# Performance work log

Hardware: AMD Instinct MI355X
Metric: run time of the kernel (lower is better)

The kernel has to match this reference:

```python
import jax, jax.numpy as jnp
import numpy as np

B, L, D_MODEL, H, H_DIM = 2, 4096, 768, 1, 128
D_K = H * H_DIM
F_LEN = L // 2 + 1
TEMP = 1.0
EPS = 1e-9
INV_SQRT_DK = float(1.0 / np.sqrt(H_DIM))


def _selector(xc, W1, b1, W2, b2, noise, temp):
    # xc: [B, h, d, F] complex. torch view_as_real(x.transpose(-1,-2))[..., 0] == real part.
    xr = jnp.real(jnp.swapaxes(xc, -1, -2))          # [B, h, F, d]
    h1 = jax.nn.relu(xr @ W1.T + b1)                 # [B, h, F, d//2]
    logit = h1 @ W2.T + b2                           # [B, h, F, 2]
    g = -jnp.log(-jnp.log(noise + EPS) + EPS)        # gumbel noise from uniform input
    z = jax.nn.softmax((logit + g) / temp, axis=-1)[..., 1]  # training mode: soft mask
    return z[..., None, :]                           # [B, h, 1, F]


def _forward(query, key, mask, Wq, bq, Wk, bk, qW1, qb1, qW2, qb2, kW1, kb1, kW2, kb2, q_noise, k_noise):
    nb, Lq = query.shape[0], query.shape[1]
    q = (query @ Wq.T + bq).reshape(nb, Lq, H, H_DIM).transpose(0, 2, 3, 1)  # [B, h, d, L]
    k = (key @ Wk.T + bk).reshape(nb, Lq, H, H_DIM).transpose(0, 2, 3, 1)
    q_tff = jnp.fft.rfft(q, axis=-1)                 # [B, h, d, F] complex
    k_tff = jnp.fft.rfft(k, axis=-1)
    q_m = _selector(q_tff, qW1, qb1, qW2, qb2, q_noise, TEMP)
    k_m = _selector(k_tff, kW1, kb1, kW2, kb2, k_noise, TEMP)
    qf = jnp.fft.irfft(q_tff * q_m, n=Lq, axis=-1)   # [B, h, d, L]
    kf = jnp.fft.irfft(k_tff * k_m, n=Lq, axis=-1)
    scores = jnp.einsum('bhdl,bhdm->bhlm', qf, kf) * INV_SQRT_DK  # [B, h, L, L]
    m = mask[:, None, :, :Lq]                        # [B, 1, 1, L]
    scores = jnp.where(m == 0, -1e9, scores)
    return jax.nn.softmax(scores, axis=-1)           # dropout omitted (eval/identity)


def setup_inputs() -> dict:
    key = jax.random.key(0)
    ks = jax.random.split(key, 12)
    s = 0.02
    return {
        'query': jax.random.normal(ks[0], (B, L, D_MODEL), jnp.float32),
        'key': jax.random.normal(ks[1], (B, L, D_MODEL), jnp.float32),
        'mask': jax.random.randint(ks[2], (B, 1, L), 0, 2, jnp.int32),
        'Wq': s * jax.random.normal(ks[3], (D_K, D_MODEL), jnp.float32),
        'bq': jnp.zeros((D_K,), jnp.float32),
        'Wk': s * jax.random.normal(ks[4], (D_K, D_MODEL), jnp.float32),
        'bk': jnp.zeros((D_K,), jnp.float32),
        'qW1': s * jax.random.normal(ks[5], (D_K // 2, D_K), jnp.float32),
        'qb1': jnp.zeros((D_K // 2,), jnp.float32),
        'qW2': s * jax.random.normal(ks[6], (2, D_K // 2), jnp.float32),
        'qb2': jnp.zeros((2,), jnp.float32),
        'kW1': s * jax.random.normal(ks[7], (D_K // 2, D_K), jnp.float32),
        'kb1': jnp.zeros((D_K // 2,), jnp.float32),
        'kW2': s * jax.random.normal(ks[8], (2, D_K // 2), jnp.float32),
        'kb2': jnp.zeros((2,), jnp.float32),
        'q_noise': jax.random.uniform(ks[9], (B, H, F_LEN, 2), jnp.float32),
        'k_noise': jax.random.uniform(ks[10], (B, H, F_LEN, 2), jnp.float32),
    }


def reference(query, key, mask, Wq, bq, Wk, bk, qW1, qb1, qW2, qb2, kW1, kb1, kW2, kb2, q_noise, k_noise):
    return _forward(query, key, mask, Wq, bq, Wk, bk, qW1, qb1, qW2, qb2, kW1, kb1, kW2, kb2, q_noise, k_noise)
```

## Files before the change

### kernel.cpp

```cpp
#include <hip/hip_runtime.h>
#include <hip/hip_bf16.h>

#define LL 4096
#define FL 2049
#define DKN 128
#define DMOD 768

#define TW_OFF   0
#define XT_OFF   4096
#define SPEC_OFF (4096 + 2097152)
#define Z_OFF    (SPEC_OFF + 2098176)

using bf16x8 = __attribute__((ext_vector_type(8))) short;
using f32x4  = __attribute__((ext_vector_type(4))) float;

__device__ __forceinline__ float2 cmul(float2 a, float2 b) {
    return make_float2(a.x * b.x - a.y * b.y, a.x * b.y + a.y * b.x);
}
__device__ __forceinline__ int SWZ(int a) { return a ^ ((a >> 4) & 15); }
__device__ __forceinline__ ushort f2bf(float f) {
    __hip_bfloat16 h = __float2bfloat16(f);
    return *(ushort*)&h;
}

__global__ void k_twiddle(float2* __restrict__ tw) {
    int j = blockIdx.x * 256 + threadIdx.x;
    if (j < 2048) {
        double a = -2.0 * 3.14159265358979323846 * (double)j / 4096.0;
        tw[j] = make_float2((float)cos(a), (float)sin(a));
    }
}

__global__ __launch_bounds__(256) void k_gemm1(const float* __restrict__ X,
                                               const float* __restrict__ W,
                                               const float* __restrict__ bias,
                                               float* __restrict__ out) {
    __shared__ float sX[16][64];
    __shared__ float sW[16][64];
    int b  = blockIdx.z;
    int l0 = blockIdx.x * 64;
    int d0 = blockIdx.y * 64;
    int t  = threadIdx.x;
    int lid = t >> 2, kq = (t & 3) * 4;
    int tx = t & 15, ty = t >> 4;
    const float* Xb = X + (size_t)b * LL * DMOD;
    float acc[4][4] = {};
    for (int k0 = 0; k0 < DMOD; k0 += 16) {
        float4 xv = *(const float4*)&Xb[(size_t)(l0 + lid) * DMOD + k0 + kq];
        float4 wv = *(const float4*)&W[(size_t)(d0 + lid) * DMOD + k0 + kq];
        sX[kq + 0][lid] = xv.x; sX[kq + 1][lid] = xv.y; sX[kq + 2][lid] = xv.z; sX[kq + 3][lid] = xv.w;
        sW[kq + 0][lid] = wv.x; sW[kq + 1][lid] = wv.y; sW[kq + 2][lid] = wv.z; sW[kq + 3][lid] = wv.w;
        __syncthreads();
#pragma unroll
        for (int k = 0; k < 16; k++) {
            float4 a = *(const float4*)&sX[k][tx * 4];
            float4 w = *(const float4*)&sW[k][ty * 4];
            acc[0][0] = fmaf(a.x, w.x, acc[0][0]); acc[0][1] = fmaf(a.x, w.y, acc[0][1]);
            acc[0][2] = fmaf(a.x, w.z, acc[0][2]); acc[0][3] = fmaf(a.x, w.w, acc[0][3]);
            acc[1][0] = fmaf(a.y, w.x, acc[1][0]); acc[1][1] = fmaf(a.y, w.y, acc[1][1]);
            acc[1][2] = fmaf(a.y, w.z, acc[1][2]); acc[1][3] = fmaf(a.y, w.w, acc[1][3]);
            acc[2][0] = fmaf(a.z, w.x, acc[2][0]); acc[2][1] = fmaf(a.z, w.y, acc[2][1]);
            acc[2][2] = fmaf(a.z, w.z, acc[2][2]); acc[2][3] = fmaf(a.z, w.w, acc[2][3]);
            acc[3][0] = fmaf(a.w, w.x, acc[3][0]); acc[3][1] = fmaf(a.w, w.y, acc[3][1]);
            acc[3][2] = fmaf(a.w, w.z, acc[3][2]); acc[3][3] = fmaf(a.w, w.w, acc[3][3]);
        }
        __syncthreads();
    }
#pragma unroll
    for (int j = 0; j < 4; j++) {
        int d = d0 + ty * 4 + j;
        float bb = bias[d];
        float4 r = make_float4(acc[0][j] + bb, acc[1][j] + bb, acc[2][j] + bb, acc[3][j] + bb);
        *(float4*)&out[((size_t)(b * DKN + d)) * LL + l0 + tx * 4] = r;
    }
}

template <int INV>
__global__ __launch_bounds__(512) void k_fft4(const float* __restrict__ xin,
                                              float2* __restrict__ spec,
                                              const float* __restrict__ zsel,
                                              float* __restrict__ xout,
                                              const float2* __restrict__ tw) {
    __shared__ float2 buf[4096];
    int ser = blockIdx.x;
    int t   = threadIdx.x;
    if (!INV) {
        const float* x = xin + (size_t)ser * LL;
        for (int i = t; i < 4096; i += 512) buf[SWZ(i)] = make_float2(x[i], 0.f);
    } else {
        const float2* sp = spec + (size_t)ser * FL;
        const float*  zz = zsel + (size_t)(ser >> 7) * FL;
        for (int f = t; f < FL; f += 512) {
            float2 v = sp[f];
            float  m = zz[f];
            float2 vm = make_float2(v.x * m, v.y * m);
            buf[SWZ(f)] = vm;
            if (f > 0 && f < 2048) buf[SWZ(4096 - f)] = make_float2(vm.x, -vm.y);
        }
    }
    __syncthreads();
#pragma unroll
    for (int st = 0; st < 6; st++) {
        int Lm1 = (1 << (2 * st)) - 1;
        float2 x0[2], x1[2], x2[2], x3[2];
#pragma unroll
        for (int ii = 0; ii < 2; ii++) {
            int idx = t + 512 * ii;
            x0[ii] = buf[SWZ(idx)];
            x1[ii] = buf[SWZ(idx + 1024)];
            x2[ii] = buf[SWZ(idx + 2048)];
            x3[ii] = buf[SWZ(idx + 3072)];
        }
        __syncthreads();
#pragma unroll
        for (int ii = 0; ii < 2; ii++) {
            int idx = t + 512 * ii;
            int q = idx & Lm1;
            int r = idx - q;
            int wbase = q + (r << 2);
            int L = Lm1 + 1;
            float2 a0 = x0[ii], a1 = x1[ii], a2 = x2[ii], a3 = x3[ii];
            float2 t0 = make_float2(a0.x + a2.x, a0.y + a2.y);
            float2 t1 = make_float2(a0.x - a2.x, a0.y - a2.y);
            float2 t2 = make_float2(a1.x + a3.x, a1.y + a3.y);
            float2 t3 = make_float2(a1.x - a3.x, a1.y - a3.y);
            float2 y0 = make_float2(t0.x + t2.x, t0.y + t2.y);
            float2 y2 = make_float2(t0.x - t2.x, t0.y - t2.y);
            float2 y1, y3;
            if (!INV) {
                y1 = make_float2(t1.x + t3.y, t1.y - t3.x);
                y3 = make_float2(t1.x - t3.y, t1.y + t3.x);
            } else {
                y1 = make_float2(t1.x - t3.y, t1.y + t3.x);
                y3 = make_float2(t1.x + t3.y, t1.y - t3.x);
            }
            float2 w1 = tw[r];
            float2 w2 = tw[2 * r];
            if (INV) { w1.y = -w1.y; w2.y = -w2.y; }
            float2 w3 = cmul(w1, w2);
            buf[SWZ(wbase)]         = y0;
            buf[SWZ(wbase + L)]     = cmul(y1, w1);
            buf[SWZ(wbase + 2 * L)] = cmul(y2, w2);
            buf[SWZ(wbase + 3 * L)] = cmul(y3, w3);
        }
        __syncthreads();
    }
    if (!INV) {
        float2* sp = spec + (size_t)ser * FL;
        for (int f = t; f < FL; f += 512) sp[f] = buf[SWZ(f)];
    } else {
        float* xo = xout + (size_t)ser * LL;
        const float sc = 1.0f / 4096.0f;
        for (int i = t; i < 4096; i += 512) xo[i] = buf[SWZ(i)].x * sc;
    }
}

__global__ __launch_bounds__(64) void k_selector(const float2* __restrict__ spec,
                                                 const float* __restrict__ W1,
                                                 const float* __restrict__ b1,
                                                 const float* __restrict__ W2,
                                                 const float* __restrict__ b2,
                                                 const float* __restrict__ noise,
                                                 float* __restrict__ z,
                                                 int tensor) {
    int f = blockIdx.x;
    int b = blockIdx.y;
    int j = threadIdx.x;
    __shared__ __align__(16) float xr[128];
    const float2* sp = spec + (size_t)(tensor * 2 + b) * DKN * FL;
    xr[j]      = sp[(size_t)j * FL + f].x;
    xr[j + 64] = sp[(size_t)(j + 64) * FL + f].x;
    __syncthreads();
    float acc = b1[j];
    const float4* w4 = (const float4*)&W1[(size_t)j * 128];
    const float4* x4 = (const float4*)xr;
#pragma unroll
    for (int d4 = 0; d4 < 32; d4++) {
        float4 w = w4[d4];
        float4 x = x4[d4];
        acc = fmaf(x.x, w.x, acc);
        acc = fmaf(x.y, w.y, acc);
        acc = fmaf(x.z, w.z, acc);
        acc = fmaf(x.w, w.w, acc);
    }
    float h = fmaxf(acc, 0.f);
    float l0 = h * W2[j];
    float l1 = h * W2[64 + j];
#pragma unroll
    for (int off = 32; off >= 1; off >>= 1) {
        l0 += __shfl_down(l0, off);
        l1 += __shfl_down(l1, off);
    }
    if (j == 0) {
        l0 += b2[0];
        l1 += b2[1];
        const float* nz = noise + ((size_t)b * FL + f) * 2;
        float g0 = -logf(-logf(nz[0] + 1e-9f) + 1e-9f);
        float g1 = -logf(-logf(nz[1] + 1e-9f) + 1e-9f);
        float a0 = l0 + g0, a1 = l1 + g1;
        z[(size_t)(tensor * 2 + b) * FL + f] = 1.f / (1.f + expf(a0 - a1));
    }
}

__global__ __launch_bounds__(256) void k_tr(const float* __restrict__ xt,
                                            ushort* __restrict__ xtb) {
    __shared__ float s[64][129];
    int tb = blockIdx.y;
    int l0 = blockIdx.x * 64;
    int t  = threadIdx.x;
    const float* g = xt + (size_t)tb * DKN * LL;
    int d = t >> 1, c0 = (t & 1) * 32;
#pragma unroll
    for (int j4 = 0; j4 < 8; j4++) {
        float4 v = *(const float4*)&g[(size_t)d * LL + l0 + c0 + j4 * 4];
        s[c0 + j4 * 4 + 0][d] = v.x;
        s[c0 + j4 * 4 + 1][d] = v.y;
        s[c0 + j4 * 4 + 2][d] = v.z;
        s[c0 + j4 * 4 + 3][d] = v.w;
    }
    __syncthreads();
    int l = t >> 2, dc0 = (t & 3) * 32;
    ushort* o = xtb + (size_t)tb * LL * DKN + (size_t)(l0 + l) * DKN + dc0;
#pragma unroll
    for (int c8 = 0; c8 < 4; c8++) {
        union { ushort us[8]; uint4 v; } pk;
#pragma unroll
        for (int u = 0; u < 8; u++) pk.us[u] = f2bf(s[l][dc0 + c8 * 8 + u]);
        *(uint4*)&o[c8 * 8] = pk.v;
    }
}

__global__ __launch_bounds__(256) void k_scores_mfma(const ushort* __restrict__ xtb,
                                                     float* __restrict__ out) {
    int b  = blockIdx.z;
    int m0 = blockIdx.x * 128;
    int l0 = blockIdx.y * 128;
    int wid  = threadIdx.x >> 6;
    int lane = threadIdx.x & 63;
    int wr = wid >> 1, wc = wid & 1;
    const ushort* A = xtb + (size_t)b * LL * DKN;
    const ushort* B = xtb + (size_t)(2 + b) * LL * DKN;
    int arow = l0 + wr * 64 + (lane & 15);
    int brow = m0 + wc * 64 + (lane & 15);
    int kcol = (lane >> 4) * 8;
    f32x4 acc[4][4] = {};
#pragma unroll
    for (int kk = 0; kk < 4; kk++) {
        bf16x8 af[4], bf[4];
#pragma unroll
        for (int mt = 0; mt < 4; mt++)
            af[mt] = *(const bf16x8*)&A[(size_t)(arow + mt * 16) * DKN + kk * 32 + kcol];
#pragma unroll
        for (int nt = 0; nt < 4; nt++)
            bf[nt] = *(const bf16x8*)&B[(size_t)(brow + nt * 16) * DKN + kk * 32 + kcol];
#pragma unroll
        for (int mt = 0; mt < 4; mt++)
#pragma unroll
            for (int nt = 0; nt < 4; nt++)
                acc[mt][nt] = __builtin_amdgcn_mfma_f32_16x16x32_bf16(af[mt], bf[nt], acc[mt][nt], 0, 0, 0);
    }
    const float sc = 0.08838834764831843f;
    int rg = lane >> 4, cl = lane & 15;
#pragma unroll
    for (int mt = 0; mt < 4; mt++) {
#pragma unroll
        for (int r = 0; r < 4; r++) {
            int l = l0 + wr * 64 + mt * 16 + rg * 4 + r;
            float* orow = out + ((size_t)(b * LL + l)) * LL + m0 + wc * 64 + cl;
#pragma unroll
            for (int nt = 0; nt < 4; nt++)
                orow[nt * 16] = acc[mt][nt][r] * sc;
        }
    }
}

__global__ __launch_bounds__(256) void k_softmax(float* __restrict__ out,
                                                 const int* __restrict__ mask) {
    int row = blockIdx.x;
    int b   = row >> 12;
    float* p = out + (size_t)row * LL;
    const int* mk = mask + (size_t)b * LL;
    int t = threadIdx.x;
    float4 v[4];
    int4   mv[4];
    float mx = -3.0e38f;
#pragma unroll
    for (int c = 0; c < 4; c++) {
        int base = c * 1024 + t * 4;
        v[c]  = *(const float4*)&p[base];
        mv[c] = *(const int4*)&mk[base];
        if (mv[c].x) mx = fmaxf(mx, v[c].x);
        if (mv[c].y) mx = fmaxf(mx, v[c].y);
        if (mv[c].z) mx = fmaxf(mx, v[c].z);
        if (mv[c].w) mx = fmaxf(mx, v[c].w);
    }
    __shared__ float redm[4], reds[4];
    int wid = t >> 6, lane = t & 63;
#pragma unroll
    for (int off = 32; off >= 1; off >>= 1) mx = fmaxf(mx, __shfl_xor(mx, off));
    if (lane == 0) redm[wid] = mx;
    __syncthreads();
    mx = fmaxf(fmaxf(redm[0], redm[1]), fmaxf(redm[2], redm[3]));
    float sum = 0.f;
#pragma unroll
    for (int c = 0; c < 4; c++) {
        v[c].x = mv[c].x ? expf(v[c].x - mx) : 0.f;
        v[c].y = mv[c].y ? expf(v[c].y - mx) : 0.f;
        v[c].z = mv[c].z ? expf(v[c].z - mx) : 0.f;
        v[c].w = mv[c].w ? expf(v[c].w - mx) : 0.f;
        sum += v[c].x + v[c].y + v[c].z + v[c].w;
    }
#pragma unroll
    for (int off = 32; off >= 1; off >>= 1) sum += __shfl_xor(sum, off);
    if (lane == 0) reds[wid] = sum;
    __syncthreads();
    sum = reds[0] + reds[1] + reds[2] + reds[3];
    float inv = 1.0f / sum;
#pragma unroll
    for (int c = 0; c < 4; c++) {
        int base = c * 1024 + t * 4;
        float4 r = make_float4(v[c].x * inv, v[c].y * inv, v[c].z * inv, v[c].w * inv);
        *(float4*)&p[base] = r;
    }
}

extern "C" void kernel_launch(void* const* d_in, const int* in_sizes, int n_in,
                              void* d_out, int out_size, void* d_ws, size_t ws_size,
                              hipStream_t stream) {
    (void)in_sizes; (void)n_in; (void)out_size; (void)ws_size;
    const float* query  = (const float*)d_in[0];
    const float* key    = (const float*)d_in[1];
    const int*   mask   = (const int*)d_in[2];
    const float* Wq     = (const float*)d_in[3];
    const float* bq     = (const float*)d_in[4];
    const float* Wk     = (const float*)d_in[5];
    const float* bk     = (const float*)d_in[6];
    const float* qW1    = (const float*)d_in[7];
    const float* qb1    = (const float*)d_in[8];
    const float* qW2    = (const float*)d_in[9];
    const float* qb2    = (const float*)d_in[10];
    const float* kW1    = (const float*)d_in[11];
    const float* kb1    = (const float*)d_in[12];
    const float* kW2    = (const float*)d_in[13];
    const float* kb2    = (const float*)d_in[14];
    const float* qnoise = (const float*)d_in[15];
    const float* knoise = (const float*)d_in[16];

    float*  ws   = (float*)d_ws;
    float2* tw   = (float2*)(ws + TW_OFF);
    float*  xt   = ws + XT_OFF;
    float2* spec = (float2*)(ws + SPEC_OFF);
    ushort* xtb  = (ushort*)(ws + SPEC_OFF);
    float*  zsel = ws + Z_OFF;
    float*  out  = (float*)d_out;

    k_twiddle<<<dim3(8), dim3(256), 0, stream>>>(tw);
    k_gemm1<<<dim3(64, 2, 2), dim3(256), 0, stream>>>(query, Wq, bq, xt);
    k_gemm1<<<dim3(64, 2, 2), dim3(256), 0, stream>>>(key, Wk, bk, xt + (size_t)2 * DKN * LL);
    k_fft4<0><<<dim3(512), dim3(512), 0, stream>>>(xt, spec, nullptr, nullptr, tw);
    k_selector<<<dim3(FL, 2), dim3(64), 0, stream>>>(spec, qW1, qb1, qW2, qb2, qnoise, zsel, 0);
    k_selector<<<dim3(FL, 2), dim3(64), 0, stream>>>(spec, kW1, kb1, kW2, kb2, knoise, zsel, 1);
    k_fft4<1><<<dim3(512), dim3(512), 0, stream>>>(nullptr, spec, zsel, xt, tw);
    k_tr<<<dim3(64, 4), dim3(256), 0, stream>>>(xt, xtb);
    k_scores_mfma<<<dim3(32, 32, 2), dim3(256), 0, stream>>>(xtb, out);
    k_softmax<<<dim3(8192), dim3(256), 0, stream>>>(out, mask);
}
```

Baseline: 404.4 us.

## Fuse scores with online softmax and use split-bf16 MFMA for projections

The QK^T score computation and the masked softmax become one kernel. It computes an online max/sum in a first pass, then recomputes the scores in a second pass and writes normalized probabilities directly. This removes the write-then-read of the full 2x4096x4096 fp32 score matrix, at the cost of doing the QK^T MFMA work twice. Separately, the fp32 input projections now run on bf16 MFMA using a hi/lo split (three products per tile), which adds conversion kernels and extra workspace traffic for the hi/lo copies.

```diff
diff --git a/kernel.cpp b/kernel.cpp
--- a/kernel.cpp
+++ b/kernel.cpp
@@ -10,6 +10,10 @@
 #define XT_OFF   4096
 #define SPEC_OFF (4096 + 2097152)
 #define Z_OFF    (SPEC_OFF + 2098176)
+#define QKH_OFF  4207624
+#define QKL_OFF  (QKH_OFF + 6291456)
+#define WH_OFF   (QKL_OFF + 6291456)
+#define WL_OFF   (WH_OFF + 98304)
 
 using bf16x8 = __attribute__((ext_vector_type(8))) short;
 using f32x4  = __attribute__((ext_vector_type(4))) float;
@@ -21,6 +25,10 @@
 __device__ __forceinline__ ushort f2bf(float f) {
     __hip_bfloat16 h = __float2bfloat16(f);
     return *(ushort*)&h;
+}
+__device__ __forceinline__ float bf2f(ushort u) {
+    __hip_bfloat16 h = *(__hip_bfloat16*)&u;
+    return __bfloat162float(h);
 }
 
 __global__ void k_twiddle(float2* __restrict__ tw) {
@@ -31,48 +39,76 @@
     }
 }
 
-__global__ __launch_bounds__(256) void k_gemm1(const float* __restrict__ X,
-                                               const float* __restrict__ W,
-                                               const float* __restrict__ bias,
-                                               float* __restrict__ out) {
-    __shared__ float sX[16][64];
-    __shared__ float sW[16][64];
-    int b  = blockIdx.z;
+__global__ __launch_bounds__(256) void k_cvt(const float* __restrict__ src,
+                                             ushort* __restrict__ hi,
+                                             ushort* __restrict__ lo, int n) {
+    int i8 = (blockIdx.x * 256 + threadIdx.x) * 8;
+    if (i8 >= n) return;
+    float4 a = *(const float4*)&src[i8];
+    float4 b = *(const float4*)&src[i8 + 4];
+    float v[8] = {a.x, a.y, a.z, a.w, b.x, b.y, b.z, b.w};
+    union { ushort us[8]; uint4 q; } ph, pl;
+#pragma unroll
+    for (int u = 0; u < 8; u++) {
+        ushort h = f2bf(v[u]);
+        ph.us[u] = h;
+        pl.us[u] = f2bf(v[u] - bf2f(h));
+    }
+    *(uint4*)&hi[i8] = ph.q;
+    *(uint4*)&lo[i8] = pl.q;
+}
+
+__global__ __launch_bounds__(256) void k_proj(const ushort* __restrict__ XH,
+                                              const ushort* __restrict__ XL,
+                                              const ushort* __restrict__ WH,
+                                              const ushort* __restrict__ WL,
+                                              const float* __restrict__ bq,
+                                              const float* __restrict__ bk,
+                                              float* __restrict__ xt) {
+    int tz = blockIdx.z, b = blockIdx.y;
     int l0 = blockIdx.x * 64;
-    int d0 = blockIdx.y * 64;
-    int t  = threadIdx.x;
-    int lid = t >> 2, kq = (t & 3) * 4;
-    int tx = t & 15, ty = t >> 4;
-    const float* Xb = X + (size_t)b * LL * DMOD;
-    float acc[4][4] = {};
-    for (int k0 = 0; k0 < DMOD; k0 += 16) {
-        float4 xv = *(const float4*)&Xb[(size_t)(l0 + lid) * DMOD + k0 + kq];
-        float4 wv = *(const float4*)&W[(size_t)(d0 + lid) * DMOD + k0 + kq];
-        sX[kq + 0][lid] = xv.x; sX[kq + 1][lid] = xv.y; sX[kq + 2][lid] = xv.z; sX[kq + 3][lid] = xv.w;
-        sW[kq + 0][lid] = wv.x; sW[kq + 1][lid] = wv.y; sW[kq + 2][lid] = wv.z; sW[kq + 3][lid] = wv.w;
-        __syncthreads();
-#pragma unroll
-        for (int k = 0; k < 16; k++) {
-            float4 a = *(const float4*)&sX[k][tx * 4];
-            float4 w = *(const float4*)&sW[k][ty * 4];
-            acc[0][0] = fmaf(a.x, w.x, acc[0][0]); acc[0][1] = fmaf(a.x, w.y, acc[0][1]);
-            acc[0][2] = fmaf(a.x, w.z, acc[0][2]); acc[0][3] = fmaf(a.x, w.w, acc[0][3]);
-            acc[1][0] = fmaf(a.y, w.x, acc[1][0]); acc[1][1] = fmaf(a.y, w.y, acc[1][1]);
-            acc[1][2] = fmaf(a.y, w.z, acc[1][2]); acc[1][3] = fmaf(a.y, w.w, acc[1][3]);
-            acc[2][0] = fmaf(a.z, w.x, acc[2][0]); acc[2][1] = fmaf(a.z, w.y, acc[2][1]);
-            acc[2][2] = fmaf(a.z, w.z, acc[2][2]); acc[2][3] = fmaf(a.z, w.w, acc[2][3]);
-            acc[3][0] = fmaf(a.w, w.x, acc[3][0]); acc[3][1] = fmaf(a.w, w.y, acc[3][1]);
-            acc[3][2] = fmaf(a.w, w.z, acc[3][2]); acc[3][3] = fmaf(a.w, w.w, acc[3][3]);
-        }
-        __syncthreads();
-    }
-#pragma unroll
-    for (int j = 0; j < 4; j++) {
-        int d = d0 + ty * 4 + j;
-        float bb = bias[d];
-        float4 r = make_float4(acc[0][j] + bb, acc[1][j] + bb, acc[2][j] + bb, acc[3][j] + bb);
-        *(float4*)&out[((size_t)(b * DKN + d)) * LL + l0 + tx * 4] = r;
-    }
+    int t = threadIdx.x, w = t >> 6, lane = t & 63;
+    int g = lane >> 4, c = lane & 15;
+    size_t xrow0 = ((size_t)(tz * 2 + b)) * LL + l0;
+    const ushort* WHt = WH + (size_t)tz * DKN * DMOD;
+    const ushort* WLt = WL + (size_t)tz * DKN * DMOD;
+    const float* bias = tz ? bk : bq;
+    float* outp = xt + (size_t)(tz * 2 + b) * DKN * LL;
+    f32x4 acc[2][4] = {};
+    for (int ks = 0; ks < 24; ks++) {
+        int kb = ks * 32 + g * 8;
+        bf16x8 ah[2], al[2], xh[4], xl[4];
+#pragma unroll
+        for (int dt = 0; dt < 2; dt++) {
+            size_t ro = (size_t)(w * 32 + dt * 16 + c) * DMOD + kb;
+            ah[dt] = *(const bf16x8*)&WHt[ro];
+            al[dt] = *(const bf16x8*)&WLt[ro];
+        }
+#pragma unroll
+        for (int nt = 0; nt < 4; nt++) {
+            size_t ro = (xrow0 + nt * 16 + c) * DMOD + kb;
+            xh[nt] = *(const bf16x8*)&XH[ro];
+            xl[nt] = *(const bf16x8*)&XL[ro];
+        }
+#pragma unroll
+        for (int dt = 0; dt < 2; dt++)
+#pragma unroll
+            for (int nt = 0; nt < 4; nt++) {
+                acc[dt][nt] = __builtin_amdgcn_mfma_f32_16x16x32_bf16(ah[dt], xh[nt], acc[dt][nt], 0, 0, 0);
+                acc[dt][nt] = __builtin_amdgcn_mfma_f32_16x16x32_bf16(ah[dt], xl[nt], acc[dt][nt], 0, 0, 0);
+                acc[dt][nt] = __builtin_amdgcn_mfma_f32_16x16x32_bf16(al[dt], xh[nt], acc[dt][nt], 0, 0, 0);
+            }
+    }
+#pragma unroll
+    for (int dt = 0; dt < 2; dt++)
+#pragma unroll
+        for (int r = 0; r < 4; r++) {
+            int d = w * 32 + dt * 16 + g * 4 + r;
+            float bd = bias[d];
+#pragma unroll
+            for (int nt = 0; nt < 4; nt++)
+                outp[(size_t)d * LL + l0 + nt * 16 + c] = acc[dt][nt][r] + bd;
+        }
 }
 
 template <int INV>
@@ -208,11 +244,11 @@
     int tb = blockIdx.y;
     int l0 = blockIdx.x * 64;
     int t  = threadIdx.x;
-    const float* g = xt + (size_t)tb * DKN * LL;
+    const float* gp = xt + (size_t)tb * DKN * LL;
     int d = t >> 1, c0 = (t & 1) * 32;
 #pragma unroll
     for (int j4 = 0; j4 < 8; j4++) {
-        float4 v = *(const float4*)&g[(size_t)d * LL + l0 + c0 + j4 * 4];
+        float4 v = *(const float4*)&gp[(size_t)d * LL + l0 + c0 + j4 * 4];
         s[c0 + j4 * 4 + 0][d] = v.x;
         s[c0 + j4 * 4 + 1][d] = v.y;
         s[c0 + j4 * 4 + 2][d] = v.z;
@@ -230,97 +266,140 @@
     }
 }
 
-__global__ __launch_bounds__(256) void k_scores_mfma(const ushort* __restrict__ xtb,
+__global__ __launch_bounds__(256) void k_scores_soft(const ushort* __restrict__ xtb,
+                                                     const int* __restrict__ mask,
                                                      float* __restrict__ out) {
-    int b  = blockIdx.z;
-    int m0 = blockIdx.x * 128;
-    int l0 = blockIdx.y * 128;
-    int wid  = threadIdx.x >> 6;
-    int lane = threadIdx.x & 63;
-    int wr = wid >> 1, wc = wid & 1;
+    int b  = blockIdx.y;
+    int l0 = blockIdx.x * 32;
+    int t = threadIdx.x, w = t >> 6, lane = t & 63;
+    int g = lane >> 4, c = lane & 15;
     const ushort* A = xtb + (size_t)b * LL * DKN;
     const ushort* B = xtb + (size_t)(2 + b) * LL * DKN;
-    int arow = l0 + wr * 64 + (lane & 15);
-    int brow = m0 + wc * 64 + (lane & 15);
-    int kcol = (lane >> 4) * 8;
-    f32x4 acc[4][4] = {};
-#pragma unroll
-    for (int kk = 0; kk < 4; kk++) {
-        bf16x8 af[4], bf[4];
-#pragma unroll
-        for (int mt = 0; mt < 4; mt++)
-            af[mt] = *(const bf16x8*)&A[(size_t)(arow + mt * 16) * DKN + kk * 32 + kcol];
-#pragma unroll
-        for (int nt = 0; nt < 4; nt++)
-            bf[nt] = *(const bf16x8*)&B[(size_t)(brow + nt * 16) * DKN + kk * 32 + kcol];
-#pragma unroll
-        for (int mt = 0; mt < 4; mt++)
+    const int* mk = mask + (size_t)b * LL;
+    const float sc = 0.08838834764831843f;
+    bf16x8 af[2][4];
+#pragma unroll
+    for (int lt = 0; lt < 2; lt++)
+#pragma unroll
+        for (int kk = 0; kk < 4; kk++)
+            af[lt][kk] = *(const bf16x8*)&A[(size_t)(l0 + lt * 16 + c) * DKN + kk * 32 + g * 8];
+    float rM[2][4], rS[2][4];
+#pragma unroll
+    for (int lt = 0; lt < 2; lt++)
+#pragma unroll
+        for (int r = 0; r < 4; r++) { rM[lt][r] = -3.0e38f; rS[lt][r] = 0.f; }
+    for (int mt = 0; mt < 16; mt++) {
+        int m0 = w * 1024 + mt * 64;
+        f32x4 acc[2][4] = {};
+#pragma unroll
+        for (int kk = 0; kk < 4; kk++) {
+            bf16x8 bfr[4];
 #pragma unroll
             for (int nt = 0; nt < 4; nt++)
-                acc[mt][nt] = __builtin_amdgcn_mfma_f32_16x16x32_bf16(af[mt], bf[nt], acc[mt][nt], 0, 0, 0);
-    }
-    const float sc = 0.08838834764831843f;
-    int rg = lane >> 4, cl = lane & 15;
-#pragma unroll
-    for (int mt = 0; mt < 4; mt++) {
+                bfr[nt] = *(const bf16x8*)&B[(size_t)(m0 + nt * 16 + c) * DKN + kk * 32 + g * 8];
+#pragma unroll
+            for (int lt = 0; lt < 2; lt++)
+#pragma unroll
+                for (int nt = 0; nt < 4; nt++)
+                    acc[lt][nt] = __builtin_amdgcn_mfma_f32_16x16x32_bf16(af[lt][kk], bfr[nt], acc[lt][nt], 0, 0, 0);
+        }
+        int mv[4];
+#pragma unroll
+        for (int nt = 0; nt < 4; nt++) mv[nt] = mk[m0 + nt * 16 + c];
+#pragma unroll
+        for (int lt = 0; lt < 2; lt++)
+#pragma unroll
+            for (int r = 0; r < 4; r++) {
+                float sv[4];
+                float vmax = -3.0e38f;
+#pragma unroll
+                for (int nt = 0; nt < 4; nt++) {
+                    float s = mv[nt] ? acc[lt][nt][r] * sc : -1.0e9f;
+                    sv[nt] = s;
+                    vmax = fmaxf(vmax, s);
+                }
+                float nm = fmaxf(rM[lt][r], vmax);
+                float ssum = 0.f;
+#pragma unroll
+                for (int nt = 0; nt < 4; nt++) ssum += __expf(sv[nt] - nm);
+                rS[lt][r] = rS[lt][r] * __expf(rM[lt][r] - nm) + ssum;
+                rM[lt][r] = nm;
+            }
+    }
+#pragma unroll
+    for (int lt = 0; lt < 2; lt++)
 #pragma unroll
         for (int r = 0; r < 4; r++) {
-            int l = l0 + wr * 64 + mt * 16 + rg * 4 + r;
-            float* orow = out + ((size_t)(b * LL + l)) * LL + m0 + wc * 64 + cl;
+            float M = rM[lt][r], S = rS[lt][r];
+#pragma unroll
+            for (int off = 1; off < 16; off <<= 1) {
+                float om = __shfl_xor(M, off);
+                float os = __shfl_xor(S, off);
+                float nm = fmaxf(M, om);
+                S = S * __expf(M - nm) + os * __expf(om - nm);
+                M = nm;
+            }
+            rM[lt][r] = M; rS[lt][r] = S;
+        }
+    __shared__ float smM[4][32], smS[4][32];
+    if (c == 0) {
+#pragma unroll
+        for (int lt = 0; lt < 2; lt++)
+#pragma unroll
+            for (int r = 0; r < 4; r++) {
+                smM[w][lt * 16 + g * 4 + r] = rM[lt][r];
+                smS[w][lt * 16 + g * 4 + r] = rS[lt][r];
+            }
+    }
+    __syncthreads();
+    float Mf[2][4], Iv[2][4];
+#pragma unroll
+    for (int lt = 0; lt < 2; lt++)
+#pragma unroll
+        for (int r = 0; r < 4; r++) {
+            int row = lt * 16 + g * 4 + r;
+            float M = -3.0e38f, S = 0.f;
+#pragma unroll
+            for (int ww = 0; ww < 4; ww++) {
+                float om = smM[ww][row];
+                float os = smS[ww][row];
+                float nm = fmaxf(M, om);
+                S = S * __expf(M - nm) + os * __expf(om - nm);
+                M = nm;
+            }
+            Mf[lt][r] = M;
+            Iv[lt][r] = 1.0f / S;
+        }
+    for (int mt = 0; mt < 16; mt++) {
+        int m0 = w * 1024 + mt * 64;
+        f32x4 acc[2][4] = {};
+#pragma unroll
+        for (int kk = 0; kk < 4; kk++) {
+            bf16x8 bfr[4];
 #pragma unroll
             for (int nt = 0; nt < 4; nt++)
-                orow[nt * 16] = acc[mt][nt][r] * sc;
-        }
-    }
-}
-
-__global__ __launch_bounds__(256) void k_softmax(float* __restrict__ out,
-                                                 const int* __restrict__ mask) {
-    int row = blockIdx.x;
-    int b   = row >> 12;
-    float* p = out + (size_t)row * LL;
-    const int* mk = mask + (size_t)b * LL;
-    int t = threadIdx.x;
-    float4 v[4];
-    int4   mv[4];
-    float mx = -3.0e38f;
-#pragma unroll
-    for (int c = 0; c < 4; c++) {
-        int base = c * 1024 + t * 4;
-        v[c]  = *(const float4*)&p[base];
-        mv[c] = *(const int4*)&mk[base];
-        if (mv[c].x) mx = fmaxf(mx, v[c].x);
-        if (mv[c].y) mx = fmaxf(mx, v[c].y);
-        if (mv[c].z) mx = fmaxf(mx, v[c].z);
-        if (mv[c].w) mx = fmaxf(mx, v[c].w);
-    }
-    __shared__ float redm[4], reds[4];
-    int wid = t >> 6, lane = t & 63;
-#pragma unroll
-    for (int off = 32; off >= 1; off >>= 1) mx = fmaxf(mx, __shfl_xor(mx, off));
-    if (lane == 0) redm[wid] = mx;
-    __syncthreads();
-    mx = fmaxf(fmaxf(redm[0], redm[1]), fmaxf(redm[2], redm[3]));
-    float sum = 0.f;
-#pragma unroll
-    for (int c = 0; c < 4; c++) {
-        v[c].x = mv[c].x ? expf(v[c].x - mx) : 0.f;
-        v[c].y = mv[c].y ? expf(v[c].y - mx) : 0.f;
-        v[c].z = mv[c].z ? expf(v[c].z - mx) : 0.f;
-        v[c].w = mv[c].w ? expf(v[c].w - mx) : 0.f;
-        sum += v[c].x + v[c].y + v[c].z + v[c].w;
-    }
-#pragma unroll
-    for (int off = 32; off >= 1; off >>= 1) sum += __shfl_xor(sum, off);
-    if (lane == 0) reds[wid] = sum;
-    __syncthreads();
-    sum = reds[0] + reds[1] + reds[2] + reds[3];
-    float inv = 1.0f / sum;
-#pragma unroll
-    for (int c = 0; c < 4; c++) {
-        int base = c * 1024 + t * 4;
-        float4 r = make_float4(v[c].x * inv, v[c].y * inv, v[c].z * inv, v[c].w * inv);
-        *(float4*)&p[base] = r;
+                bfr[nt] = *(const bf16x8*)&B[(size_t)(m0 + nt * 16 + c) * DKN + kk * 32 + g * 8];
+#pragma unroll
+            for (int lt = 0; lt < 2; lt++)
+#pragma unroll
+                for (int nt = 0; nt < 4; nt++)
+                    acc[lt][nt] = __builtin_amdgcn_mfma_f32_16x16x32_bf16(af[lt][kk], bfr[nt], acc[lt][nt], 0, 0, 0);
+        }
+        int mv[4];
+#pragma unroll
+        for (int nt = 0; nt < 4; nt++) mv[nt] = mk[m0 + nt * 16 + c];
+#pragma unroll
+        for (int lt = 0; lt < 2; lt++)
+#pragma unroll
+            for (int r = 0; r < 4; r++) {
+                int l = l0 + lt * 16 + g * 4 + r;
+                float* orow = out + ((size_t)(b * LL + l)) * LL;
+#pragma unroll
+                for (int nt = 0; nt < 4; nt++) {
+                    float s = mv[nt] ? acc[lt][nt][r] * sc : -1.0e9f;
+                    orow[m0 + nt * 16 + c] = __expf(s - Mf[lt][r]) * Iv[lt][r];
+                }
+            }
     }
 }
 
@@ -352,16 +431,25 @@
     float2* spec = (float2*)(ws + SPEC_OFF);
     ushort* xtb  = (ushort*)(ws + SPEC_OFF);
     float*  zsel = ws + Z_OFF;
+    ushort* qkh  = (ushort*)(ws + QKH_OFF);
+    ushort* qkl  = (ushort*)(ws + QKL_OFF);
+    ushort* wh   = (ushort*)(ws + WH_OFF);
+    ushort* wl   = (ushort*)(ws + WL_OFF);
     float*  out  = (float*)d_out;
 
+    const int NQK = 2 * LL * DMOD;
+    const int NW  = DKN * DMOD;
+
     k_twiddle<<<dim3(8), dim3(256), 0, stream>>>(tw);
-    k_gemm1<<<dim3(64, 2, 2), dim3(256), 0, stream>>>(query, Wq, bq, xt);
-    k_gemm1<<<dim3(64, 2, 2), dim3(256), 0, stream>>>(key, Wk, bk, xt + (size_t)2 * DKN * LL);
+    k_cvt<<<dim3(NQK / 2048), dim3(256), 0, stream>>>(query, qkh, qkl, NQK);
+    k_cvt<<<dim3(NQK / 2048), dim3(256), 0, stream>>>(key, qkh + NQK, qkl + NQK, NQK);
+    k_cvt<<<dim3(NW / 2048), dim3(256), 0, stream>>>(Wq, wh, wl, NW);
+    k_cvt<<<dim3(NW / 2048), dim3(256), 0, stream>>>(Wk, wh + NW, wl + NW, NW);
+    k_proj<<<dim3(64, 2, 2), dim3(256), 0, stream>>>(qkh, qkl, wh, wl, bq, bk, xt);
     k_fft4<0><<<dim3(512), dim3(512), 0, stream>>>(xt, spec, nullptr, nullptr, tw);
     k_selector<<<dim3(FL, 2), dim3(64), 0, stream>>>(spec, qW1, qb1, qW2, qb2, qnoise, zsel, 0);
     k_selector<<<dim3(FL, 2), dim3(64), 0, stream>>>(spec, kW1, kb1, kW2, kb2, knoise, zsel, 1);
     k_fft4<1><<<dim3(512), dim3(512), 0, stream>>>(nullptr, spec, zsel, xt, tw);
     k_tr<<<dim3(64, 4), dim3(256), 0, stream>>>(xt, xtb);
-    k_scores_mfma<<<dim3(32, 32, 2), dim3(256), 0, stream>>>(xtb, out);
-    k_softmax<<<dim3(8192), dim3(256), 0, stream>>>(out, mask);
-}
+    k_scores_soft<<<dim3(128, 2), dim3(256), 0, stream>>>(xtb, mask, out);
+}
```

Result: no change. 407.1 us (+0.6%).
